# Performance work log

Hardware: AMD Instinct MI355X
Metric: run time of the kernel (lower is better)

## Reference

```python
import jax, jax.numpy as jnp
import numpy as np

N_VERT = 20000


def _gather_pad(feat, adj):
    # feat: [B, N, C]; adj: [B, N, K] with 1-based indices, 0 = padding (-> zeros)
    B, N, C = feat.shape
    padded = jnp.concatenate([jnp.zeros((B, 1, C), feat.dtype), feat], axis=1)  # [B, N+1, C]
    return jax.vmap(lambda p, a: p[a])(padded, adj)  # [B, N, K, C]


def setup_inputs() -> dict:
    key = jax.random.key(0)
    ks = jax.random.split(key, 7)
    B, N, K, M, C, O = 4, N_VERT, 16, 9, 64, 64
    x = jax.random.normal(ks[0], (B, N, C), jnp.float32)
    adj = jax.random.randint(ks[1], (B, N, K), 0, N + 1, jnp.int32)  # 0 == no neighbor
    W = jax.random.normal(ks[2], (M, O, C), jnp.float32) * 0.1
    b = jax.random.normal(ks[3], (O,), jnp.float32) * 0.1
    u = jax.random.normal(ks[4], (M, C), jnp.float32) * 0.1
    v = jax.random.normal(ks[5], (M, C), jnp.float32) * 0.1
    c = jax.random.normal(ks[6], (M,), jnp.float32) * 0.1
    return {"x": x, "adj": adj, "W": W, "b": b, "u": u, "v": v, "c": c}


def reference(x, adj, W, b, u, v, c):
    # FEAST graph conv, non-invariant path.
    mask = adj != 0  # [B, N, K]
    # attention logits: u.x_i + v.x_j + c, masked (padding) neighbors -> 0 + c
    ux = jnp.einsum('bnc,mc->bnm', x, u)          # [B, N, M]
    vx = jnp.einsum('bnc,mc->bnm', x, v)          # [B, N, M]
    vxn = _gather_pad(vx, adj)                    # [B, N, K, M]
    logits = jnp.where(mask[..., None], ux[:, :, None, :] + vxn, 0.0) + c
    q = jax.nn.softmax(logits, axis=-1)           # softmax over M kernels
    # gather raw neighbor features (zero for padding), contract q over K first,
    # then apply per-kernel W (linear, so order is equivalent to original wx-gather)
    xn = _gather_pad(x, adj)                      # [B, N, K, C]
    s = jnp.einsum('bnkm,bnkc->bnmc', q, xn)      # [B, N, M, C]
    out = jnp.einsum('bnmc,moc->bno', s, W)       # [B, N, O]
    deg = jnp.sum(mask, axis=-1).astype(x.dtype)  # [B, N]
    inv_deg = jnp.where(deg > 0, 1.0 / jnp.maximum(deg, 1.0), 0.0)
    return out * inv_deg[..., None] + b
```

## Files before the change

### kernel.cpp

```cpp
#include <hip/hip_runtime.h>
#include <cstdint>
#include <cstddef>

#define BB 4
#define NN 20000
#define KK 16
#define MM 9
#define CC 64
#define OO 64
#define BN (BB*NN)
#define MC (MM*CC)
#define UVP 12
#define QNP 160
#define SCP 72
#define SNP (MM*SCP)
#define NKS (MC/32)

typedef _Float16 f16x8 __attribute__((ext_vector_type(8)));
typedef _Float16 f16x4 __attribute__((ext_vector_type(4)));
typedef __fp16   fp16v2 __attribute__((ext_vector_type(2)));
typedef float    f32x4 __attribute__((ext_vector_type(4)));
typedef unsigned short u16;
typedef unsigned int   u32;

union Hcv { _Float16 h; u16 u; };
__device__ __forceinline__ u16 f2h(float f) { Hcv t; t.h = (_Float16)f; return t.u; }
__device__ __forceinline__ float h2f(u16 h) { Hcv t; t.u = h; return (float)t.h; }

__global__ __launch_bounds__(256) void setup_kernel(
    const float* __restrict__ x, const float* __restrict__ W,
    const float* __restrict__ u, const float* __restrict__ v,
    u16* __restrict__ xh, u16* __restrict__ wfb2,
    u16* __restrict__ Gh, u16* __restrict__ Gl)
{
    int bid = blockIdx.x;
    if (bid < 5000) {
        int i = bid * 1024 + threadIdx.x * 4;
        float4 xv = *(const float4*)(x + i);
        ushort4 hv;
        hv.x = f2h(xv.x); hv.y = f2h(xv.y); hv.z = f2h(xv.z); hv.w = f2h(xv.w);
        *(ushort4*)(xh + i) = hv;
    } else if (bid < 5144) {
        int i = (bid - 5000) * 256 + threadIdx.x;
        int j = i & 7, o = (i >> 3) & 63, lhi = (i >> 9) & 3, ks = i >> 11;
        int kf = ks * 32 + lhi * 8 + j;
        int m = kf >> 6, cc = kf & 63;
        wfb2[i] = f2h(W[m * 4096 + o * 64 + cc]);
    } else {
        int i = (bid - 5144) * 256 + threadIdx.x;
        int r = i >> 6, cc = i & 63;
        float val = (r < 9) ? u[r * 64 + cc] : ((r < 18) ? v[(r - 9) * 64 + cc] : 0.f);
        u16 h = f2h(val);
        Gh[i] = h;
        Gl[i] = f2h(val - h2f(h));
    }
}

__global__ __launch_bounds__(256) void uxvx_kernel(
    const float* __restrict__ x,
    const u16* __restrict__ Gh, const u16* __restrict__ Gl,
    const float* __restrict__ c, float* __restrict__ uxc, float* __restrict__ vxp)
{
    const int wave = threadIdx.x >> 6, lane = threadIdx.x & 63;
    const int lr = lane & 15, lhi = lane >> 4;
    const int t0 = blockIdx.x * 64 + wave * 16;

    const float* xr = x + (size_t)(t0 + lr) * 64 + lhi * 8;
    float xf[16];
    *(float4*)(xf + 0)  = *(const float4*)(xr + 0);
    *(float4*)(xf + 4)  = *(const float4*)(xr + 4);
    *(float4*)(xf + 8)  = *(const float4*)(xr + 32);
    *(float4*)(xf + 12) = *(const float4*)(xr + 36);
    union { u16 us[8]; f16x8 v; } H0, L0, H1, L1;
    #pragma unroll
    for (int i = 0; i < 8; ++i) {
        u16 h = f2h(xf[i]);      H0.us[i] = h; L0.us[i] = f2h(xf[i] - h2f(h));
        u16 h2 = f2h(xf[8 + i]); H1.us[i] = h2; L1.us[i] = f2h(xf[8 + i] - h2f(h2));
    }

    f32x4 acc0 = {0.f,0.f,0.f,0.f}, acc1 = {0.f,0.f,0.f,0.f};
    #pragma unroll
    for (int t = 0; t < 2; ++t) {
        f32x4 acc = {0.f,0.f,0.f,0.f};
        #pragma unroll
        for (int s = 0; s < 2; ++s) {
            f16x8 gh = *(const f16x8*)(Gh + (t * 16 + lr) * 64 + s * 32 + lhi * 8);
            f16x8 gl = *(const f16x8*)(Gl + (t * 16 + lr) * 64 + s * 32 + lhi * 8);
            f16x8 as  = s ? H1.v : H0.v;
            f16x8 asl = s ? L1.v : L0.v;
            acc = __builtin_amdgcn_mfma_f32_16x16x32_f16(as,  gh, acc, 0, 0, 0);
            acc = __builtin_amdgcn_mfma_f32_16x16x32_f16(as,  gl, acc, 0, 0, 0);
            acc = __builtin_amdgcn_mfma_f32_16x16x32_f16(asl, gh, acc, 0, 0, 0);
        }
        if (t == 0) acc0 = acc; else acc1 = acc;
    }

    float cv = (lr < 9) ? c[lr] : 0.f;
    #pragma unroll
    for (int reg = 0; reg < 4; ++reg) {
        int node = t0 + lhi * 4 + reg;
        if (lr < 9) uxc[(size_t)node * UVP + lr] = acc0[reg] + cv;
        else        vxp[(size_t)node * UVP + (lr - 9)] = acc0[reg];
        if (lr < 2) vxp[(size_t)node * UVP + 7 + lr] = acc1[reg];
    }
}

__global__ __launch_bounds__(256) void fused_kernel(
    const u16* __restrict__ xh, const int* __restrict__ adj,
    const float* __restrict__ uxc, const float* __restrict__ vxp,
    const u16* __restrict__ wfb2, const float* __restrict__ bias,
    float* __restrict__ out)
{
    __shared__ __align__(16) u16 qlds[16 * QNP + 96];
    __shared__ __align__(16) u16 slds[16 * SNP];
    const int tid = threadIdx.x, wave = tid >> 6, lane = tid & 63;
    const int lr = lane & 15, lhi = lane >> 4;
    const int node0 = blockIdx.x * 16;
    const int b = node0 / NN;
    const int rowbase = b * NN;

    const int g = lhi;
    const int k = lr;
    const int node = node0 + wave * 4 + g;
    int jj = adj[(size_t)node0 * KK + tid];
    unsigned long long bal = __ballot(jj != 0);
    int deg = __popcll((bal >> (g * 16)) & 0xffffull);
    float inv = (deg > 0) ? (1.0f / (float)deg) : 0.0f;

    float q[MM];
    #pragma unroll
    for (int m = 0; m < MM; ++m) q[m] = 0.f;
    if (jj != 0) {
        const float4* ur = (const float4*)(uxc + (size_t)node * UVP);
        const float4* vr = (const float4*)(vxp + ((size_t)rowbase + (jj - 1)) * UVP);
        float4 u0 = ur[0], u1 = ur[1], u2 = ur[2];
        float4 v0 = vr[0], v1 = vr[1], v2 = vr[2];
        float l[MM] = { u0.x+v0.x, u0.y+v0.y, u0.z+v0.z, u0.w+v0.w,
                        u1.x+v1.x, u1.y+v1.y, u1.z+v1.z, u1.w+v1.w,
                        u2.x+v2.x };
        float mx = l[0];
        #pragma unroll
        for (int m = 1; m < MM; ++m) mx = fmaxf(mx, l[m]);
        float sum = 0.f;
        #pragma unroll
        for (int m = 0; m < MM; ++m) { l[m] = __expf(l[m] - mx); sum += l[m]; }
        float sc = inv / sum;
        #pragma unroll
        for (int m = 0; m < MM; ++m) q[m] = l[m] * sc;
    }
    {
        u16* qw = qlds + (wave * 4 + g) * QNP + k;
        #pragma unroll
        for (int m = 0; m < MM; ++m) qw[m * 16] = f2h(q[m]);
    }

    f16x8 idf[2];
    #pragma unroll
    for (int s = 0; s < 2; ++s) {
        union { u16 us[8]; f16x8 v; } t;
        #pragma unroll
        for (int j = 0; j < 8; ++j)
            t.us[j] = (lhi * 8 + j == s * 16 + lr) ? (u16)0x3C00 : (u16)0;
        idf[s] = t.v;
    }

    const u16* xhb = xh + ((size_t)rowbase << 6);
    f16x8 aLo[4], aHi[4];
    f16x4 qf[4];
    #pragma unroll
    for (int g2 = 0; g2 < 4; ++g2) {
        int e = __builtin_amdgcn_ds_bpermute((g2 * 16 + lr) * 4, jj);
        int erow = ((e > 0) ? e : 1) - 1;
        const u16* rp = xhb + ((size_t)erow << 6) + lhi * 8;
        aLo[g2] = *(const f16x8*)(rp);
        aHi[g2] = *(const f16x8*)(rp + 32);
        qf[g2]  = *(const f16x4*)(qlds + (wave * 4 + g2) * QNP + lr * 16 + lhi * 4);
    }

    #pragma unroll
    for (int g2 = 0; g2 < 4; ++g2) {
        const int rnode = wave * 4 + g2;
        const int swz = ((rnode >> 3) & 1) * 32;
        #pragma unroll
        for (int cc = 0; cc < 4; ++cc) {
            f32x4 xt = {0.f,0.f,0.f,0.f};
            xt = __builtin_amdgcn_mfma_f32_16x16x32_f16(
                     (cc < 2) ? aLo[g2] : aHi[g2], idf[cc & 1], xt, 0, 0, 0);
            union { fp16v2 h2[2]; f16x4 h4; } at;
            at.h2[0] = __builtin_amdgcn_cvt_pkrtz(xt[0], xt[1]);
            at.h2[1] = __builtin_amdgcn_cvt_pkrtz(xt[2], xt[3]);
            f32x4 d2 = {0.f,0.f,0.f,0.f};
            d2 = __builtin_amdgcn_mfma_f32_16x16x16f16(at.h4, qf[g2], d2, 0, 0, 0);
            if (lr < 9) {
                u32 lo = __builtin_amdgcn_perm((u32)f2h(d2[1]), (u32)f2h(d2[0]), 0x05040100u);
                u32 hi = __builtin_amdgcn_perm((u32)f2h(d2[3]), (u32)f2h(d2[2]), 0x05040100u);
                uint2* p = (uint2*)(slds + rnode * SNP + lr * SCP
                                    + ((cc * 16 + lhi * 4) ^ swz));
                *p = make_uint2(lo, hi);
            }
        }
    }
    __syncthreads();

    const int o0 = wave * 16;
    const int swzR = ((lr >> 3) & 1) * 32;
    f32x4 acc = {0.f,0.f,0.f,0.f};
    #pragma unroll
    for (int ks = 0; ks < NKS; ++ks) {
        int kf = ks * 32 + lhi * 8;
        int m = kf >> 6, coff = kf & 63;
        f16x8 afrag = *(const f16x8*)(slds + lr * SNP + m * SCP + (coff ^ swzR));
        f16x8 bfrag = *(const f16x8*)(wfb2 + (size_t)(((ks * 4 + lhi) * 64) + o0 + lr) * 8);
        acc = __builtin_amdgcn_mfma_f32_16x16x32_f16(afrag, bfrag, acc, 0, 0, 0);
    }
    float bv = bias[o0 + lr];
    #pragma unroll
    for (int reg = 0; reg < 4; ++reg) {
        int rr = node0 + lhi * 4 + reg;
        out[(size_t)rr * OO + o0 + lr] = acc[reg] + bv;
    }
}

extern "C" void kernel_launch(void* const* d_in, const int* in_sizes, int n_in,
                              void* d_out, int out_size, void* d_ws, size_t ws_size,
                              hipStream_t stream)
{
    const float* x   = (const float*)d_in[0];
    const int*   adj = (const int*)  d_in[1];
    const float* W   = (const float*)d_in[2];
    const float* b   = (const float*)d_in[3];
    const float* u   = (const float*)d_in[4];
    const float* v   = (const float*)d_in[5];
    const float* c   = (const float*)d_in[6];
    float* out = (float*)d_out;

    float* uxc = (float*)d_ws;
    float* vxp = uxc + (size_t)BN * UVP;
    u16*   xh  = (u16*)(vxp + (size_t)BN * UVP);
    u16*   wfb2= xh + (size_t)BN * CC;
    u16*   Gh  = wfb2 + (size_t)NKS * 2048;
    u16*   Gl  = Gh + 2048;

    setup_kernel<<<5152, 256, 0, stream>>>(x, W, u, v, xh, wfb2, Gh, Gl);
    uxvx_kernel<<<1250, 256, 0, stream>>>(x, Gh, Gl, c, uxc, vxp);
    fused_kernel<<<5000, 256, 0, stream>>>(xh, adj, uxc, vxp, wfb2, b, out);
}
```

Measured before the change: 139.0 us.

## Merge setup and uxvx kernels; process 32 nodes per fused block with prefetch

Folds the x-to-fp16 conversion, W repacking and u/v hi/lo splitting into the uxvx kernel, which removes one launch and the x re-read as well as the Gh/Gl buffers. The fused kernel now handles two 16-node groups per block, issuing the second group's gathers before the first group's output GEMM so that global latency overlaps compute. It also halves the grid and drops the LDS swizzle, which may bring back bank conflicts and adds a barrier and register pressure.

Result: faster. 133.6 us (-3.9%).

```diff
diff --git a/kernel.cpp b/kernel.cpp
--- a/kernel.cpp
+++ b/kernel.cpp
@@ -11,7 +11,7 @@
 #define BN (BB*NN)
 #define MC (MM*CC)
 #define UVP 12
-#define QNP 160
+#define QNP 272
 #define SCP 72
 #define SNP (MM*SCP)
 #define NKS (MC/32)
@@ -27,78 +27,81 @@
 __device__ __forceinline__ u16 f2h(float f) { Hcv t; t.h = (_Float16)f; return t.u; }
 __device__ __forceinline__ float h2f(u16 h) { Hcv t; t.u = h; return (float)t.h; }
 
-__global__ __launch_bounds__(256) void setup_kernel(
+__global__ __launch_bounds__(256) void pre_kernel(
     const float* __restrict__ x, const float* __restrict__ W,
     const float* __restrict__ u, const float* __restrict__ v,
-    u16* __restrict__ xh, u16* __restrict__ wfb2,
-    u16* __restrict__ Gh, u16* __restrict__ Gl)
+    const float* __restrict__ c,
+    float* __restrict__ uxc, float* __restrict__ vxp,
+    u16* __restrict__ xh, u16* __restrict__ wfb2)
 {
-    int bid = blockIdx.x;
-    if (bid < 5000) {
-        int i = bid * 1024 + threadIdx.x * 4;
-        float4 xv = *(const float4*)(x + i);
-        ushort4 hv;
-        hv.x = f2h(xv.x); hv.y = f2h(xv.y); hv.z = f2h(xv.z); hv.w = f2h(xv.w);
-        *(ushort4*)(xh + i) = hv;
-    } else if (bid < 5144) {
-        int i = (bid - 5000) * 256 + threadIdx.x;
-        int j = i & 7, o = (i >> 3) & 63, lhi = (i >> 9) & 3, ks = i >> 11;
-        int kf = ks * 32 + lhi * 8 + j;
-        int m = kf >> 6, cc = kf & 63;
-        wfb2[i] = f2h(W[m * 4096 + o * 64 + cc]);
-    } else {
-        int i = (bid - 5144) * 256 + threadIdx.x;
-        int r = i >> 6, cc = i & 63;
-        float val = (r < 9) ? u[r * 64 + cc] : ((r < 18) ? v[(r - 9) * 64 + cc] : 0.f);
-        u16 h = f2h(val);
-        Gh[i] = h;
-        Gl[i] = f2h(val - h2f(h));
-    }
-}
-
-__global__ __launch_bounds__(256) void uxvx_kernel(
-    const float* __restrict__ x,
-    const u16* __restrict__ Gh, const u16* __restrict__ Gl,
-    const float* __restrict__ c, float* __restrict__ uxc, float* __restrict__ vxp)
-{
+    const int bid = blockIdx.x;
+    if (bid >= 1250) {
+        int base = (bid - 1250) * 1024 + threadIdx.x * 4;
+        ushort4 wv;
+        u16* wp = (u16*)&wv;
+        #pragma unroll
+        for (int t = 0; t < 4; ++t) {
+            int i = base + t;
+            int j = i & 7, o = (i >> 3) & 63, l2 = (i >> 9) & 3, ks = i >> 11;
+            int kf = ks * 32 + l2 * 8 + j;
+            int m = kf >> 6, cc2 = kf & 63;
+            wp[t] = f2h(W[m * 4096 + o * 64 + cc2]);
+        }
+        *(ushort4*)(wfb2 + base) = wv;
+        return;
+    }
     const int wave = threadIdx.x >> 6, lane = threadIdx.x & 63;
     const int lr = lane & 15, lhi = lane >> 4;
-    const int t0 = blockIdx.x * 64 + wave * 16;
-
-    const float* xr = x + (size_t)(t0 + lr) * 64 + lhi * 8;
+    const int t0n = bid * 64 + wave * 16;
+
+    const float* xr = x + (size_t)(t0n + lr) * 64 + lhi * 8;
     float xf[16];
     *(float4*)(xf + 0)  = *(const float4*)(xr + 0);
     *(float4*)(xf + 4)  = *(const float4*)(xr + 4);
     *(float4*)(xf + 8)  = *(const float4*)(xr + 32);
     *(float4*)(xf + 12) = *(const float4*)(xr + 36);
-    union { u16 us[8]; f16x8 v; } H0, L0, H1, L1;
+    union { u16 us[8]; f16x8 v; ushort4 s4[2]; } H0, L0, H1, L1;
     #pragma unroll
     for (int i = 0; i < 8; ++i) {
-        u16 h = f2h(xf[i]);      H0.us[i] = h; L0.us[i] = f2h(xf[i] - h2f(h));
+        u16 h = f2h(xf[i]);      H0.us[i] = h;  L0.us[i] = f2h(xf[i] - h2f(h));
         u16 h2 = f2h(xf[8 + i]); H1.us[i] = h2; L1.us[i] = f2h(xf[8 + i] - h2f(h2));
     }
+    *(ushort4*)(xh + (size_t)(t0n + lr) * 64 + lhi * 8)      = H0.s4[0];
+    *(ushort4*)(xh + (size_t)(t0n + lr) * 64 + lhi * 8 + 4)  = H0.s4[1];
+    *(ushort4*)(xh + (size_t)(t0n + lr) * 64 + 32 + lhi * 8)     = H1.s4[0];
+    *(ushort4*)(xh + (size_t)(t0n + lr) * 64 + 32 + lhi * 8 + 4) = H1.s4[1];
 
     f32x4 acc0 = {0.f,0.f,0.f,0.f}, acc1 = {0.f,0.f,0.f,0.f};
     #pragma unroll
     for (int t = 0; t < 2; ++t) {
+        int r = t * 16 + lr;
+        const float* gp = (r < 9) ? (u + r * 64) : (v + (r - 9) * 64);
+        bool nz = r < 18;
         f32x4 acc = {0.f,0.f,0.f,0.f};
         #pragma unroll
         for (int s = 0; s < 2; ++s) {
-            f16x8 gh = *(const f16x8*)(Gh + (t * 16 + lr) * 64 + s * 32 + lhi * 8);
-            f16x8 gl = *(const f16x8*)(Gl + (t * 16 + lr) * 64 + s * 32 + lhi * 8);
+            float gf[8];
+            *(float4*)(gf + 0) = nz ? *(const float4*)(gp + s * 32 + lhi * 8)
+                                    : make_float4(0.f,0.f,0.f,0.f);
+            *(float4*)(gf + 4) = nz ? *(const float4*)(gp + s * 32 + lhi * 8 + 4)
+                                    : make_float4(0.f,0.f,0.f,0.f);
+            union { u16 us[8]; f16x8 v; } GH, GL;
+            #pragma unroll
+            for (int i = 0; i < 8; ++i) {
+                u16 h = f2h(gf[i]); GH.us[i] = h; GL.us[i] = f2h(gf[i] - h2f(h));
+            }
             f16x8 as  = s ? H1.v : H0.v;
             f16x8 asl = s ? L1.v : L0.v;
-            acc = __builtin_amdgcn_mfma_f32_16x16x32_f16(as,  gh, acc, 0, 0, 0);
-            acc = __builtin_amdgcn_mfma_f32_16x16x32_f16(as,  gl, acc, 0, 0, 0);
-            acc = __builtin_amdgcn_mfma_f32_16x16x32_f16(asl, gh, acc, 0, 0, 0);
+            acc = __builtin_amdgcn_mfma_f32_16x16x32_f16(as,  GH.v, acc, 0, 0, 0);
+            acc = __builtin_amdgcn_mfma_f32_16x16x32_f16(as,  GL.v, acc, 0, 0, 0);
+            acc = __builtin_amdgcn_mfma_f32_16x16x32_f16(asl, GH.v, acc, 0, 0, 0);
         }
         if (t == 0) acc0 = acc; else acc1 = acc;
     }
-
     float cv = (lr < 9) ? c[lr] : 0.f;
     #pragma unroll
     for (int reg = 0; reg < 4; ++reg) {
-        int node = t0 + lhi * 4 + reg;
+        int node = t0n + lhi * 4 + reg;
         if (lr < 9) uxc[(size_t)node * UVP + lr] = acc0[reg] + cv;
         else        vxp[(size_t)node * UVP + (lr - 9)] = acc0[reg];
         if (lr < 2) vxp[(size_t)node * UVP + 7 + lr] = acc1[reg];
@@ -111,45 +114,49 @@
     const u16* __restrict__ wfb2, const float* __restrict__ bias,
     float* __restrict__ out)
 {
-    __shared__ __align__(16) u16 qlds[16 * QNP + 96];
+    __shared__ __align__(16) u16 qlds[32 * QNP];
     __shared__ __align__(16) u16 slds[16 * SNP];
     const int tid = threadIdx.x, wave = tid >> 6, lane = tid & 63;
     const int lr = lane & 15, lhi = lane >> 4;
-    const int node0 = blockIdx.x * 16;
+    const int node0 = blockIdx.x * 32;
     const int b = node0 / NN;
     const int rowbase = b * NN;
+    const u16* xhb = xh + ((size_t)rowbase << 6);
 
     const int g = lhi;
     const int k = lr;
-    const int node = node0 + wave * 4 + g;
-    int jj = adj[(size_t)node0 * KK + tid];
-    unsigned long long bal = __ballot(jj != 0);
-    int deg = __popcll((bal >> (g * 16)) & 0xffffull);
-    float inv = (deg > 0) ? (1.0f / (float)deg) : 0.0f;
-
-    float q[MM];
-    #pragma unroll
-    for (int m = 0; m < MM; ++m) q[m] = 0.f;
-    if (jj != 0) {
-        const float4* ur = (const float4*)(uxc + (size_t)node * UVP);
-        const float4* vr = (const float4*)(vxp + ((size_t)rowbase + (jj - 1)) * UVP);
-        float4 u0 = ur[0], u1 = ur[1], u2 = ur[2];
-        float4 v0 = vr[0], v1 = vr[1], v2 = vr[2];
-        float l[MM] = { u0.x+v0.x, u0.y+v0.y, u0.z+v0.z, u0.w+v0.w,
-                        u1.x+v1.x, u1.y+v1.y, u1.z+v1.z, u1.w+v1.w,
-                        u2.x+v2.x };
-        float mx = l[0];
-        #pragma unroll
-        for (int m = 1; m < MM; ++m) mx = fmaxf(mx, l[m]);
-        float sum = 0.f;
-        #pragma unroll
-        for (int m = 0; m < MM; ++m) { l[m] = __expf(l[m] - mx); sum += l[m]; }
-        float sc = inv / sum;
-        #pragma unroll
-        for (int m = 0; m < MM; ++m) q[m] = l[m] * sc;
-    }
-    {
-        u16* qw = qlds + (wave * 4 + g) * QNP + k;
+    int jjA[2];
+    jjA[0] = adj[(size_t)node0 * KK + tid];
+    jjA[1] = adj[(size_t)node0 * KK + 256 + tid];
+    #pragma unroll
+    for (int t = 0; t < 2; ++t) {
+        int jj = jjA[t];
+        unsigned long long bal = __ballot(jj != 0);
+        int deg = __popcll((bal >> (g * 16)) & 0xffffull);
+        float inv = (deg > 0) ? (1.0f / (float)deg) : 0.0f;
+        const int node = node0 + t * 16 + wave * 4 + g;
+        float q[MM];
+        #pragma unroll
+        for (int m = 0; m < MM; ++m) q[m] = 0.f;
+        if (jj != 0) {
+            const float4* ur = (const float4*)(uxc + (size_t)node * UVP);
+            const float4* vr = (const float4*)(vxp + ((size_t)rowbase + (jj - 1)) * UVP);
+            float4 u0 = ur[0], u1 = ur[1], u2 = ur[2];
+            float4 v0 = vr[0], v1 = vr[1], v2 = vr[2];
+            float l[MM] = { u0.x+v0.x, u0.y+v0.y, u0.z+v0.z, u0.w+v0.w,
+                            u1.x+v1.x, u1.y+v1.y, u1.z+v1.z, u1.w+v1.w,
+                            u2.x+v2.x };
+            float mx = l[0];
+            #pragma unroll
+            for (int m = 1; m < MM; ++m) mx = fmaxf(mx, l[m]);
+            float sum = 0.f;
+            #pragma unroll
+            for (int m = 0; m < MM; ++m) { l[m] = __expf(l[m] - mx); sum += l[m]; }
+            float sc = inv / sum;
+            #pragma unroll
+            for (int m = 0; m < MM; ++m) q[m] = l[m] * sc;
+        }
+        u16* qw = qlds + (t * 16 + wave * 4 + g) * QNP + k;
         #pragma unroll
         for (int m = 0; m < MM; ++m) qw[m * 16] = f2h(q[m]);
     }
@@ -164,12 +171,11 @@
         idf[s] = t.v;
     }
 
-    const u16* xhb = xh + ((size_t)rowbase << 6);
     f16x8 aLo[4], aHi[4];
     f16x4 qf[4];
     #pragma unroll
     for (int g2 = 0; g2 < 4; ++g2) {
-        int e = __builtin_amdgcn_ds_bpermute((g2 * 16 + lr) * 4, jj);
+        int e = __builtin_amdgcn_ds_bpermute((g2 * 16 + lr) * 4, jjA[0]);
         int erow = ((e > 0) ? e : 1) - 1;
         const u16* rp = xhb + ((size_t)erow << 6) + lhi * 8;
         aLo[g2] = *(const f16x8*)(rp);
@@ -180,7 +186,6 @@
     #pragma unroll
     for (int g2 = 0; g2 < 4; ++g2) {
         const int rnode = wave * 4 + g2;
-        const int swz = ((rnode >> 3) & 1) * 32;
         #pragma unroll
         for (int cc = 0; cc < 4; ++cc) {
             f32x4 xt = {0.f,0.f,0.f,0.f};
@@ -194,30 +199,83 @@
             if (lr < 9) {
                 u32 lo = __builtin_amdgcn_perm((u32)f2h(d2[1]), (u32)f2h(d2[0]), 0x05040100u);
                 u32 hi = __builtin_amdgcn_perm((u32)f2h(d2[3]), (u32)f2h(d2[2]), 0x05040100u);
-                uint2* p = (uint2*)(slds + rnode * SNP + lr * SCP
-                                    + ((cc * 16 + lhi * 4) ^ swz));
+                uint2* p = (uint2*)(slds + rnode * SNP + lr * SCP + cc * 16 + lhi * 4);
                 *p = make_uint2(lo, hi);
             }
         }
     }
     __syncthreads();
 
+    f16x8 bLo[4], bHi[4];
+    f16x4 qg[4];
+    #pragma unroll
+    for (int g2 = 0; g2 < 4; ++g2) {
+        int e = __builtin_amdgcn_ds_bpermute((g2 * 16 + lr) * 4, jjA[1]);
+        int erow = ((e > 0) ? e : 1) - 1;
+        const u16* rp = xhb + ((size_t)erow << 6) + lhi * 8;
+        bLo[g2] = *(const f16x8*)(rp);
+        bHi[g2] = *(const f16x8*)(rp + 32);
+        qg[g2]  = *(const f16x4*)(qlds + (16 + wave * 4 + g2) * QNP + lr * 16 + lhi * 4);
+    }
+
     const int o0 = wave * 16;
-    const int swzR = ((lr >> 3) & 1) * 32;
-    f32x4 acc = {0.f,0.f,0.f,0.f};
-    #pragma unroll
-    for (int ks = 0; ks < NKS; ++ks) {
-        int kf = ks * 32 + lhi * 8;
-        int m = kf >> 6, coff = kf & 63;
-        f16x8 afrag = *(const f16x8*)(slds + lr * SNP + m * SCP + (coff ^ swzR));
-        f16x8 bfrag = *(const f16x8*)(wfb2 + (size_t)(((ks * 4 + lhi) * 64) + o0 + lr) * 8);
-        acc = __builtin_amdgcn_mfma_f32_16x16x32_f16(afrag, bfrag, acc, 0, 0, 0);
-    }
     float bv = bias[o0 + lr];
-    #pragma unroll
-    for (int reg = 0; reg < 4; ++reg) {
-        int rr = node0 + lhi * 4 + reg;
-        out[(size_t)rr * OO + o0 + lr] = acc[reg] + bv;
+    {
+        f32x4 acc = {0.f,0.f,0.f,0.f};
+        #pragma unroll
+        for (int ks = 0; ks < NKS; ++ks) {
+            int kf = ks * 32 + lhi * 8;
+            int m = kf >> 6, coff = kf & 63;
+            f16x8 afrag = *(const f16x8*)(slds + lr * SNP + m * SCP + coff);
+            f16x8 bfrag = *(const f16x8*)(wfb2 + (size_t)(((ks * 4 + lhi) * 64) + o0 + lr) * 8);
+            acc = __builtin_amdgcn_mfma_f32_16x16x32_f16(afrag, bfrag, acc, 0, 0, 0);
+        }
+        #pragma unroll
+        for (int reg = 0; reg < 4; ++reg) {
+            int rr = node0 + lhi * 4 + reg;
+            out[(size_t)rr * OO + o0 + lr] = acc[reg] + bv;
+        }
+    }
+    __syncthreads();
+
+    #pragma unroll
+    for (int g2 = 0; g2 < 4; ++g2) {
+        const int rnode = wave * 4 + g2;
+        #pragma unroll
+        for (int cc = 0; cc < 4; ++cc) {
+            f32x4 xt = {0.f,0.f,0.f,0.f};
+            xt = __builtin_amdgcn_mfma_f32_16x16x32_f16(
+                     (cc < 2) ? bLo[g2] : bHi[g2], idf[cc & 1], xt, 0, 0, 0);
+            union { fp16v2 h2[2]; f16x4 h4; } at;
+            at.h2[0] = __builtin_amdgcn_cvt_pkrtz(xt[0], xt[1]);
+            at.h2[1] = __builtin_amdgcn_cvt_pkrtz(xt[2], xt[3]);
+            f32x4 d2 = {0.f,0.f,0.f,0.f};
+            d2 = __builtin_amdgcn_mfma_f32_16x16x16f16(at.h4, qg[g2], d2, 0, 0, 0);
+            if (lr < 9) {
+                u32 lo = __builtin_amdgcn_perm((u32)f2h(d2[1]), (u32)f2h(d2[0]), 0x05040100u);
+                u32 hi = __builtin_amdgcn_perm((u32)f2h(d2[3]), (u32)f2h(d2[2]), 0x05040100u);
+                uint2* p = (uint2*)(slds + rnode * SNP + lr * SCP + cc * 16 + lhi * 4);
+                *p = make_uint2(lo, hi);
+            }
+        }
+    }
+    __syncthreads();
+
+    {
+        f32x4 acc = {0.f,0.f,0.f,0.f};
+        #pragma unroll
+        for (int ks = 0; ks < NKS; ++ks) {
+            int kf = ks * 32 + lhi * 8;
+            int m = kf >> 6, coff = kf & 63;
+            f16x8 afrag = *(const f16x8*)(slds + lr * SNP + m * SCP + coff);
+            f16x8 bfrag = *(const f16x8*)(wfb2 + (size_t)(((ks * 4 + lhi) * 64) + o0 + lr) * 8);
+            acc = __builtin_amdgcn_mfma_f32_16x16x32_f16(afrag, bfrag, acc, 0, 0, 0);
+        }
+        #pragma unroll
+        for (int reg = 0; reg < 4; ++reg) {
+            int rr = node0 + 16 + lhi * 4 + reg;
+            out[(size_t)rr * OO + o0 + lr] = acc[reg] + bv;
+        }
     }
 }
 
@@ -238,10 +296,7 @@
     float* vxp = uxc + (size_t)BN * UVP;
     u16*   xh  = (u16*)(vxp + (size_t)BN * UVP);
     u16*   wfb2= xh + (size_t)BN * CC;
-    u16*   Gh  = wfb2 + (size_t)NKS * 2048;
-    u16*   Gl  = Gh + 2048;
-
-    setup_kernel<<<5152, 256, 0, stream>>>(x, W, u, v, xh, wfb2, Gh, Gl);
-    uxvx_kernel<<<1250, 256, 0, stream>>>(x, Gh, Gl, c, uxc, vxp);
-    fused_kernel<<<5000, 256, 0, stream>>>(xh, adj, uxc, vxp, wfb2, b, out);
+
+    pre_kernel<<<1286, 256, 0, stream>>>(x, W, u, v, c, uxc, vxp, xh, wfb2);
+    fused_kernel<<<2500, 256, 0, stream>>>(xh, adj, uxc, vxp, wfb2, b, out);
 }
```
